# Optimization experiments

Measured on AMD Instinct MI355X. Metric: run time of the kernel, lower is better.

Reference implementation:

```python
import jax, jax.numpy as jnp
import numpy as np
import math

S, B, D, H = 2048, 2, 1024, 16
DK = D // H


def setup_inputs() -> dict:
    key = jax.random.key(0)
    ks = jax.random.split(key, 13)
    scale = 1.0 / math.sqrt(D)
    inp = {
        "query": jax.random.normal(ks[0], (S, B, D), jnp.float32),
        "key": jax.random.normal(ks[1], (S, B, D), jnp.float32),
        "value": jax.random.normal(ks[2], (S, B, D), jnp.float32),
        "mask": jax.random.normal(ks[3], (B, S, S), jnp.float32),
        # four Linear(d_model, d_model) layers: q, k, v, out. torch convention W:(out,in)
        "Wq": jax.random.normal(ks[4], (D, D), jnp.float32) * scale,
        "bq": jax.random.normal(ks[5], (D,), jnp.float32) * scale,
        "Wk": jax.random.normal(ks[6], (D, D), jnp.float32) * scale,
        "bk": jax.random.normal(ks[7], (D,), jnp.float32) * scale,
        "Wv": jax.random.normal(ks[8], (D, D), jnp.float32) * scale,
        "bv": jax.random.normal(ks[9], (D,), jnp.float32) * scale,
        "Wo": jax.random.normal(ks[10], (D, D), jnp.float32) * scale,
        "bo": jax.random.normal(ks[11], (D,), jnp.float32) * scale,
    }
    return inp


def reference(query, key, value, mask, Wq, bq, Wk, bk, Wv, bv, Wo, bo):
    # inputs are (tokens S, batch B, d_model D)
    def proj(x, W, b):  # torch Linear: x @ W.T + b, then split heads -> (B,H,S,DK)
        y = jnp.einsum('sbd,ed->sbe', x, W) + b
        return y.reshape(S, B, H, DK).transpose(1, 2, 0, 3)

    q = proj(query, Wq, bq)
    k = proj(key, Wk, bk)
    v = proj(value, Wv, bv)

    scores = jnp.einsum('bhsd,bhtd->bhst', q, k) / math.sqrt(DK)
    scores = scores + mask[:, None, :, :]  # broadcast over heads
    p_attn = jax.nn.softmax(scores, axis=-1)  # (B,H,S,S)

    x = jnp.einsum('bhst,bhtd->bhsd', p_attn, v)  # (B,H,S,DK)
    x = x.transpose(2, 0, 1, 3).reshape(S, B, D)  # (S,B,D)
    out = jnp.einsum('sbd,ed->sbe', x, Wo) + bo

    attn = p_attn.mean(axis=1)  # mean over heads -> (B,S,S)
    return out, attn
```

## Files before the change

kernel.cpp:

```cpp
#include <hip/hip_runtime.h>
#include <hip/hip_bf16.h>


#define S_LEN 2048
#define BATCH 2
#define DMODEL 1024
#define NH 16
#define DKH 64
#define SCALE 0.125f
#define QSCALE 0.180336878f
#define FMAX 20.0f
#define KSTRIDE 72

typedef __bf16 bf16_t;
typedef __attribute__((ext_vector_type(8))) __bf16 bf16x8;
typedef __attribute__((ext_vector_type(8))) unsigned short u16x8;
typedef __attribute__((ext_vector_type(4))) unsigned short u16x4;
typedef __attribute__((ext_vector_type(4))) float f32x4;

__device__ __forceinline__ unsigned short f32_bf16_rne(float f) {
  union { float f; unsigned int u; } v; v.f = f;
  unsigned int u = v.u;
  u += 0x7fffu + ((u >> 16) & 1u);
  return (unsigned short)(u >> 16);
}
__device__ __forceinline__ float bf16u_f32(unsigned short us) {
  union { unsigned int u; float f; } v; v.u = ((unsigned int)us) << 16;
  return v.f;
}
__device__ __forceinline__ f32x4 mfma_bf16(bf16x8 a, bf16x8 b, f32x4 c) {
  return __builtin_amdgcn_mfma_f32_16x16x32_bf16(a, b, c, 0, 0, 0);
}
__device__ __forceinline__ float exp2_fast(float x) {
#if __has_builtin(__builtin_amdgcn_exp2f)
  return __builtin_amdgcn_exp2f(x);
#else
  return __expf(x * 0.69314718f);
#endif
}
__device__ __forceinline__ unsigned int cvtpk(float lo, float hi) {
  unsigned int r;
  asm("v_cvt_pk_bf16_f32 %0, %1, %2" : "=v"(r) : "v"(lo), "v"(hi));
  return r;
}
__device__ __forceinline__ void gload16(const bf16_t* g, unsigned short* l) {
  __builtin_amdgcn_global_load_lds(
      (const __attribute__((address_space(1))) void*)g,
      (__attribute__((address_space(3))) void*)l, 16, 0, 0);
}

__global__ __launch_bounds__(256) void cvt_w_kernel(
    const float* __restrict__ w0, const float* __restrict__ w1,
    const float* __restrict__ w2, const float* __restrict__ w3,
    bf16_t* __restrict__ o0, bf16_t* __restrict__ o1,
    bf16_t* __restrict__ o2, bf16_t* __restrict__ o3) {
  const float* src; bf16_t* dst;
  switch (blockIdx.y) {
    case 0: src = w0; dst = o0; break;
    case 1: src = w1; dst = o1; break;
    case 2: src = w2; dst = o2; break;
    default: src = w3; dst = o3; break;
  }
  int i = (blockIdx.x * 256 + threadIdx.x) * 4;
  float4 v = *(const float4*)(src + i);
  union { unsigned short u[4]; uint2 q; } r;
  r.u[0] = f32_bf16_rne(v.x); r.u[1] = f32_bf16_rne(v.y);
  r.u[2] = f32_bf16_rne(v.z); r.u[3] = f32_bf16_rne(v.w);
  *(uint2*)(dst + i) = r.q;
}

__global__ __launch_bounds__(256) void cvt_x_kernel(
    const float* __restrict__ x0, const float* __restrict__ x1,
    const float* __restrict__ x2,
    bf16_t* __restrict__ o0, bf16_t* __restrict__ o1, bf16_t* __restrict__ o2) {
  const float* src; bf16_t* dst;
  switch (blockIdx.y) {
    case 0: src = x0; dst = o0; break;
    case 1: src = x1; dst = o1; break;
    default: src = x2; dst = o2; break;
  }
  int i = (blockIdx.x * 256 + threadIdx.x) * 4;
  float4 v = *(const float4*)(src + i);
  union { unsigned short u[4]; uint2 q; } r;
  r.u[0] = f32_bf16_rne(v.x); r.u[1] = f32_bf16_rne(v.y);
  r.u[2] = f32_bf16_rne(v.z); r.u[3] = f32_bf16_rne(v.w);
  *(uint2*)(dst + i) = r.q;
}

__global__ __launch_bounds__(256) void cvt_mask_kernel(
    const float* __restrict__ m, bf16_t* __restrict__ o) {
  int i = (blockIdx.x * 256 + threadIdx.x) * 4;
  float4 v = *(const float4*)(m + i);
  union { unsigned short u[4]; uint2 q; } r;
  r.u[0] = f32_bf16_rne(__expf(v.x - FMAX));
  r.u[1] = f32_bf16_rne(__expf(v.y - FMAX));
  r.u[2] = f32_bf16_rne(__expf(v.z - FMAX));
  r.u[3] = f32_bf16_rne(__expf(v.w - FMAX));
  *(uint2*)(o + i) = r.q;
}

__global__ __launch_bounds__(256) void proj_kernel(
    const bf16_t* __restrict__ Xq, const bf16_t* __restrict__ Xk, const bf16_t* __restrict__ Xv,
    const bf16_t* __restrict__ Wqb, const bf16_t* __restrict__ Wkb, const bf16_t* __restrict__ Wvb,
    const float* __restrict__ bq, const float* __restrict__ bk, const float* __restrict__ bv,
    bf16_t* __restrict__ qo, bf16_t* __restrict__ ko, bf16_t* __restrict__ vTo) {
  int mode = blockIdx.z;
  const bf16_t* X = (mode == 0) ? Xq : (mode == 1) ? Xk : Xv;
  const bf16_t* W = (mode == 0) ? Wqb : (mode == 1) ? Wkb : Wvb;
  const float* bias = (mode == 0) ? bq : (mode == 1) ? bk : bv;

  __shared__ __align__(16) unsigned short Alds[128 * 32];
  __shared__ __align__(16) unsigned short Blds[128 * 32];

  int tid = threadIdx.x;
  int wv = tid >> 6, lane = tid & 63, quad = lane >> 4, col = lane & 15;
  int wr = wv >> 1, wc = wv & 1;
  int rowbase = blockIdx.x * 128;
  int colbase = blockIdx.y * 128;

  int srow = tid >> 2;
  int sk8 = (tid & 3) * 8;
  const bf16_t* ga0 = X + (size_t)(rowbase + srow) * DMODEL + sk8;
  const bf16_t* gb0 = W + (size_t)(colbase + srow) * DMODEL + sk8;
  unsigned short* la0 = Alds + tid * 8;
  unsigned short* lb0 = Blds + tid * 8;

  f32x4 acc[4][4] = {};

  for (int k0 = 0; k0 < DMODEL; k0 += 32) {
    gload16(ga0 + k0, la0);
    gload16(ga0 + 64 * DMODEL + k0, la0 + 2048);
    gload16(gb0 + k0, lb0);
    gload16(gb0 + 64 * DMODEL + k0, lb0 + 2048);
    __syncthreads();

    union { u16x8 u; bf16x8 v; } af[4], bfr[4];
#pragma unroll
    for (int mi = 0; mi < 4; ++mi)
      af[mi].u = *(const u16x8*)(Alds + (wr * 64 + mi * 16 + col) * 32 + quad * 8);
#pragma unroll
    for (int ni = 0; ni < 4; ++ni)
      bfr[ni].u = *(const u16x8*)(Blds + (wc * 64 + ni * 16 + col) * 32 + quad * 8);
#pragma unroll
    for (int mi = 0; mi < 4; ++mi)
#pragma unroll
      for (int ni = 0; ni < 4; ++ni)
        acc[mi][ni] = mfma_bf16(af[mi].v, bfr[ni].v, acc[mi][ni]);
    __syncthreads();
  }

  float biasv[4];
#pragma unroll
  for (int ni = 0; ni < 4; ++ni)
    biasv[ni] = bias[colbase + wc * 64 + ni * 16 + col];

#pragma unroll
  for (int mi = 0; mi < 4; ++mi)
#pragma unroll
    for (int ni = 0; ni < 4; ++ni)
#pragma unroll
      for (int r = 0; r < 4; ++r) {
        int grow = rowbase + wr * 64 + mi * 16 + quad * 4 + r;
        int gcol = colbase + wc * 64 + ni * 16 + col;
        float val = acc[mi][ni][r] + biasv[ni];
        if (mode == 0) val *= QSCALE;
        unsigned short us = f32_bf16_rne(val);
        int s = grow >> 1, bb = grow & 1;
        int h = gcol >> 6, dk = gcol & 63;
        if (mode == 2) {
          ((unsigned short*)vTo)[((size_t)(bb * NH + h) * DKH + dk) * S_LEN + s] = us;
        } else {
          unsigned short* dst = (unsigned short*)(mode == 0 ? qo : ko);
          dst[((size_t)(bb * NH + h) * S_LEN + s) * DKH + dk] = us;
        }
      }
}

__global__ __launch_bounds__(256) void flash_kernel(
    const bf16_t* __restrict__ emb,
    const bf16_t* __restrict__ q_ws, const bf16_t* __restrict__ k_ws,
    const bf16_t* __restrict__ vT_ws,
    bf16_t* __restrict__ x_ws, float* __restrict__ rl_ws) {
  int tid = threadIdx.x;
  int w = tid >> 6, lane = tid & 63, quad = lane >> 4, col = lane & 15;

  int bid = blockIdx.x;
  int wi = bid >> 3;
  int bh = (bid & 7) * 4 + (wi & 3);
  int qblk = wi >> 2;
  int b = bh >> 4;
  int s0 = qblk * 128 + w * 32;
  int sA = s0, sB = s0 + 16;

  __shared__ __align__(16) unsigned short Klds[64 * KSTRIDE];
  __shared__ __align__(16) unsigned short Vlds[64 * KSTRIDE];

  const bf16_t* qh = q_ws + (size_t)bh * S_LEN * DKH;
  const bf16_t* kh = k_ws + (size_t)bh * S_LEN * DKH;
  const bf16_t* vh = vT_ws + (size_t)bh * DKH * S_LEN;
  const unsigned short* emA = (const unsigned short*)emb +
      (size_t)b * S_LEN * S_LEN + (size_t)(sA + col) * S_LEN;
  const unsigned short* emB = emA + (size_t)16 * S_LEN;

  bf16x8 qA0 = *(const bf16x8*)(qh + (sA + col) * DKH + quad * 8);
  bf16x8 qA1 = *(const bf16x8*)(qh + (sA + col) * DKH + 32 + quad * 8);
  bf16x8 qB0 = *(const bf16x8*)(qh + (sB + col) * DKH + quad * 8);
  bf16x8 qB1 = *(const bf16x8*)(qh + (sB + col) * DKH + 32 + quad * 8);

  int row1 = tid >> 3, row2 = row1 + 32;
  int ch = (tid & 7) * 8;
  int pi1 = (row1 & 32) + ((row1 & 16) >> 2) + ((row1 & 12) << 1) + (row1 & 3);
  int pi2 = (row2 & 32) + ((row2 & 16) >> 2) + ((row2 & 12) << 1) + (row2 & 3);
  const unsigned short* kg1 = (const unsigned short*)kh + (size_t)pi1 * DKH + ch;
  const unsigned short* kg2 = (const unsigned short*)kh + (size_t)pi2 * DKH + ch;
  const unsigned short* vg1 = (const unsigned short*)vh + (size_t)row1 * S_LEN + ch;
  const unsigned short* vg2 = (const unsigned short*)vh + (size_t)row2 * S_LEN + ch;
  u16x8* kl1 = (u16x8*)(Klds + row1 * KSTRIDE + ch);
  u16x8* kl2 = (u16x8*)(Klds + row2 * KSTRIDE + ch);
  u16x8* vl1 = (u16x8*)(Vlds + row1 * KSTRIDE + ch);
  u16x8* vl2 = (u16x8*)(Vlds + row2 * KSTRIDE + ch);

  f32x4 xA[4] = {}, xB[4] = {};
  float lsumA = 0.0f, lsumB = 0.0f;

  u16x8 kp1 = *(const u16x8*)kg1;
  u16x8 kp2 = *(const u16x8*)kg2;
  u16x8 vp1 = *(const u16x8*)vg1;
  u16x8 vp2 = *(const u16x8*)vg2;

  for (int t0 = 0; t0 < S_LEN; t0 += 64) {
    *kl1 = kp1; *kl2 = kp2; *vl1 = vp1; *vl2 = vp2;
    __syncthreads();

    if (t0 + 64 < S_LEN) {
      kp1 = *(const u16x8*)(kg1 + (size_t)(t0 + 64) * DKH);
      kp2 = *(const u16x8*)(kg2 + (size_t)(t0 + 64) * DKH);
      vp1 = *(const u16x8*)(vg1 + (t0 + 64));
      vp2 = *(const u16x8*)(vg2 + (t0 + 64));
    }

    u16x4 emA4[4], emB4[4];
#pragma unroll
    for (int j = 0; j < 4; ++j) {
      int f = t0 + ((j >> 1) << 5) + ((j & 1) << 2) + quad * 8;
      emA4[j] = *(const u16x4*)(emA + f);
      emB4[j] = *(const u16x4*)(emB + f);
    }

    f32x4 CA[4], CB[4];
#pragma unroll
    for (int j = 0; j < 4; ++j) {
      union { u16x8 u; bf16x8 v; } kb0, kb1;
      int row = j * 16 + col;
      kb0.u = *(const u16x8*)(Klds + row * KSTRIDE + quad * 8);
      kb1.u = *(const u16x8*)(Klds + row * KSTRIDE + 32 + quad * 8);
      f32x4 z = {};
      CA[j] = mfma_bf16(kb1.v, qA1, mfma_bf16(kb0.v, qA0, z));
      CB[j] = mfma_bf16(kb1.v, qB1, mfma_bf16(kb0.v, qB0, z));
    }

    unsigned int PA[8], PB[8];
#pragma unroll
    for (int j = 0; j < 4; ++j) {
      float a0 = exp2_fast(CA[j][0]) * bf16u_f32(emA4[j][0]);
      float a1 = exp2_fast(CA[j][1]) * bf16u_f32(emA4[j][1]);
      float a2 = exp2_fast(CA[j][2]) * bf16u_f32(emA4[j][2]);
      float a3 = exp2_fast(CA[j][3]) * bf16u_f32(emA4[j][3]);
      lsumA += (a0 + a1) + (a2 + a3);
      PA[j * 2] = cvtpk(a0, a1);
      PA[j * 2 + 1] = cvtpk(a2, a3);
      float b0 = exp2_fast(CB[j][0]) * bf16u_f32(emB4[j][0]);
      float b1 = exp2_fast(CB[j][1]) * bf16u_f32(emB4[j][1]);
      float b2 = exp2_fast(CB[j][2]) * bf16u_f32(emB4[j][2]);
      float b3 = exp2_fast(CB[j][3]) * bf16u_f32(emB4[j][3]);
      lsumB += (b0 + b1) + (b2 + b3);
      PB[j * 2] = cvtpk(b0, b1);
      PB[j * 2 + 1] = cvtpk(b2, b3);
    }
    union { unsigned int u32[4]; bf16x8 v; } bA0, bA1, bB0, bB1;
#pragma unroll
    for (int i = 0; i < 4; ++i) {
      bA0.u32[i] = PA[i]; bA1.u32[i] = PA[4 + i];
      bB0.u32[i] = PB[i]; bB1.u32[i] = PB[4 + i];
    }

#pragma unroll
    for (int ni = 0; ni < 4; ++ni) {
      union { u16x8 u; bf16x8 v; } vb0, vb1;
      int row = ni * 16 + col;
      vb0.u = *(const u16x8*)(Vlds + row * KSTRIDE + quad * 8);
      vb1.u = *(const u16x8*)(Vlds + row * KSTRIDE + 32 + quad * 8);
      xA[ni] = mfma_bf16(vb1.v, bA1.v, mfma_bf16(vb0.v, bA0.v, xA[ni]));
      xB[ni] = mfma_bf16(vb1.v, bB1.v, mfma_bf16(vb0.v, bB0.v, xB[ni]));
    }
    __syncthreads();
  }

  lsumA += __shfl_xor(lsumA, 16, 64); lsumA += __shfl_xor(lsumA, 32, 64);
  lsumB += __shfl_xor(lsumB, 16, 64); lsumB += __shfl_xor(lsumB, 32, 64);
  float rlA = 1.0f / lsumA, rlB = 1.0f / lsumB;

  unsigned short* xo = (unsigned short*)x_ws;
#pragma unroll
  for (int ni = 0; ni < 4; ++ni) {
    uint2 wa, wb;
    wa.x = cvtpk(xA[ni][0] * rlA, xA[ni][1] * rlA);
    wa.y = cvtpk(xA[ni][2] * rlA, xA[ni][3] * rlA);
    wb.x = cvtpk(xB[ni][0] * rlB, xB[ni][1] * rlB);
    wb.y = cvtpk(xB[ni][2] * rlB, xB[ni][3] * rlB);
    *(uint2*)(xo + ((size_t)bh * S_LEN + sA + col) * DKH + ni * 16 + quad * 4) = wa;
    *(uint2*)(xo + ((size_t)bh * S_LEN + sB + col) * DKH + ni * 16 + quad * 4) = wb;
  }
  if (quad == 0) {
    rl_ws[(size_t)bh * S_LEN + sA + col] = rlA;
    rl_ws[(size_t)bh * S_LEN + sB + col] = rlB;
  }
}

__global__ __launch_bounds__(512) void attn_kernel(
    const bf16_t* __restrict__ emb,
    const bf16_t* __restrict__ q_ws, const bf16_t* __restrict__ k_ws,
    const float* __restrict__ rl_ws,
    float* __restrict__ attn_out) {
  int tid = threadIdx.x;
  int w = tid >> 6, lane = tid & 63, quad = lane >> 4, col = lane & 15;
  int b = blockIdx.y;
  int s0 = blockIdx.x * 128 + w * 16;
  int t_base = blockIdx.z * 128;

  __shared__ __align__(16) unsigned short Klds[2][128 * 64];

  const unsigned short* emrow = (const unsigned short*)emb +
      (size_t)b * S_LEN * S_LEN + (size_t)(s0 + quad * 4) * S_LEN + t_base;
  float emf[8][4];
#pragma unroll
  for (int j = 0; j < 8; ++j)
#pragma unroll
    for (int r = 0; r < 4; ++r)
      emf[j][r] = bf16u_f32(emrow[r * S_LEN + j * 16 + col]);

  int srow = tid >> 3;
  int csw = ((tid & 7) ^ (srow & 7)) * 8;
  const bf16_t* kh0 = k_ws + (size_t)(b * NH) * S_LEN * DKH;
  const bf16_t* ks1 = kh0 + (size_t)(t_base + srow) * DKH + csw;
  const bf16_t* ks2 = kh0 + (size_t)(t_base + 64 + srow) * DKH + csw;

  const bf16_t* qp0 = q_ws + (size_t)(b * NH) * S_LEN * DKH + (size_t)(s0 + col) * DKH;
  const float* rlp = rl_ws + (size_t)(b * NH) * S_LEN + s0 + quad * 4;

  f32x4 acc[8] = {};

  gload16(ks1, &Klds[0][0] + tid * 8);
  gload16(ks2, &Klds[0][0] + 4096 + tid * 8);
  bf16x8 qf0c = *(const bf16x8*)(qp0 + quad * 8);
  bf16x8 qf1c = *(const bf16x8*)(qp0 + 32 + quad * 8);
  float rlc[4];
#pragma unroll
  for (int r = 0; r < 4; ++r) rlc[r] = rlp[r];
  __syncthreads();

  int cur = 0;
  for (int h = 0; h < NH; ++h) {
    bf16x8 qf0n = qf0c, qf1n = qf1c;
    float rln[4] = {rlc[0], rlc[1], rlc[2], rlc[3]};
    if (h + 1 < NH) {
      size_t off = (size_t)(h + 1) * S_LEN * DKH;
      unsigned short* dn = &Klds[cur ^ 1][0];
      gload16(ks1 + off, dn + tid * 8);
      gload16(ks2 + off, dn + 4096 + tid * 8);
      qf0n = *(const bf16x8*)(qp0 + off + quad * 8);
      qf1n = *(const bf16x8*)(qp0 + off + 32 + quad * 8);
      const float* rlh = rlp + (size_t)(h + 1) * S_LEN;
#pragma unroll
      for (int r = 0; r < 4; ++r) rln[r] = rlh[r];
    }

    const unsigned short* kb = &Klds[cur][0];
#pragma unroll
    for (int j = 0; j < 8; ++j) {
      int row = j * 16 + col;
      int rsw = row & 7;
      union { u16x8 u; bf16x8 v; } kb0, kb1;
      kb0.u = *(const u16x8*)(kb + row * 64 + ((quad ^ rsw) << 3));
      kb1.u = *(const u16x8*)(kb + row * 64 + (((quad + 4) ^ rsw) << 3));
      f32x4 z = {};
      f32x4 C = mfma_bf16(qf1c, kb1.v, mfma_bf16(qf0c, kb0.v, z));
#pragma unroll
      for (int r = 0; r < 4; ++r)
        acc[j][r] = fmaf(exp2_fast(C[r]), rlc[r], acc[j][r]);
    }
    __syncthreads();
    cur ^= 1;
    qf0c = qf0n; qf1c = qf1n;
#pragma unroll
    for (int r = 0; r < 4; ++r) rlc[r] = rln[r];
  }

#pragma unroll
  for (int j = 0; j < 8; ++j)
#pragma unroll
    for (int r = 0; r < 4; ++r)
      attn_out[((size_t)b * S_LEN + s0 + quad * 4 + r) * S_LEN + t_base + j * 16 + col] =
          acc[j][r] * emf[j][r] * (1.0f / NH);
}

__global__ __launch_bounds__(256) void outproj_kernel(
    const bf16_t* __restrict__ x_ws, const bf16_t* __restrict__ Wob,
    const float* __restrict__ bo, float* __restrict__ out) {
  __shared__ __align__(16) unsigned short Alds[128 * 32];
  __shared__ __align__(16) unsigned short Blds[128 * 32];

  int tid = threadIdx.x;
  int wv = tid >> 6, lane = tid & 63, quad = lane >> 4, col = lane & 15;
  int wr = wv >> 1, wc = wv & 1;
  int rowbase = blockIdx.x * 128;
  int colbase = blockIdx.y * 128;

  int srow = tid >> 2;
  int sk8 = (tid & 3) * 8;
  int r0 = rowbase + srow;
  int s0a = r0 >> 1, b0a = r0 & 1;
  int r1 = r0 + 64;
  int s1a = r1 >> 1, b1a = r1 & 1;
  const bf16_t* gb0 = Wob + (size_t)(colbase + srow) * DMODEL + sk8;
  unsigned short* la0 = Alds + tid * 8;
  unsigned short* lb0 = Blds + tid * 8;

  f32x4 acc[4][4] = {};

  for (int k0 = 0; k0 < DMODEL; k0 += 32) {
    int h = k0 >> 6, dk = (k0 & 63) + sk8;
    gload16(x_ws + ((size_t)(b0a * NH + h) * S_LEN + s0a) * DKH + dk, la0);
    gload16(x_ws + ((size_t)(b1a * NH + h) * S_LEN + s1a) * DKH + dk, la0 + 2048);
    gload16(gb0 + k0, lb0);
    gload16(gb0 + 64 * DMODEL + k0, lb0 + 2048);
    __syncthreads();

    union { u16x8 u; bf16x8 v; } af[4], bfr[4];
#pragma unroll
    for (int mi = 0; mi < 4; ++mi)
      af[mi].u = *(const u16x8*)(Alds + (wr * 64 + mi * 16 + col) * 32 + quad * 8);
#pragma unroll
    for (int ni = 0; ni < 4; ++ni)
      bfr[ni].u = *(const u16x8*)(Blds + (wc * 64 + ni * 16 + col) * 32 + quad * 8);
#pragma unroll
    for (int mi = 0; mi < 4; ++mi)
#pragma unroll
      for (int ni = 0; ni < 4; ++ni)
        acc[mi][ni] = mfma_bf16(af[mi].v, bfr[ni].v, acc[mi][ni]);
    __syncthreads();
  }

  float biasv[4];
#pragma unroll
  for (int ni = 0; ni < 4; ++ni)
    biasv[ni] = bo[colbase + wc * 64 + ni * 16 + col];

#pragma unroll
  for (int mi = 0; mi < 4; ++mi)
#pragma unroll
    for (int ni = 0; ni < 4; ++ni)
#pragma unroll
      for (int r = 0; r < 4; ++r) {
        int grow = rowbase + wr * 64 + mi * 16 + quad * 4 + r;
        int gcol = colbase + wc * 64 + ni * 16 + col;
        out[(size_t)grow * DMODEL + gcol] = acc[mi][ni][r] + biasv[ni];
      }
}

extern "C" void kernel_launch(void* const* d_in, const int* in_sizes, int n_in,
                              void* d_out, int out_size, void* d_ws, size_t ws_size,
                              hipStream_t stream) {
  const float* query = (const float*)d_in[0];
  const float* key_  = (const float*)d_in[1];
  const float* value = (const float*)d_in[2];
  const float* mask  = (const float*)d_in[3];
  const float* Wq = (const float*)d_in[4];
  const float* bq = (const float*)d_in[5];
  const float* Wk = (const float*)d_in[6];
  const float* bk = (const float*)d_in[7];
  const float* Wv = (const float*)d_in[8];
  const float* bv = (const float*)d_in[9];
  const float* Wo = (const float*)d_in[10];
  const float* bo = (const float*)d_in[11];

  char* ws = (char*)d_ws;
  bf16_t* q_ws  = (bf16_t*)(ws + 0);
  bf16_t* k_ws  = (bf16_t*)(ws + 8388608);
  bf16_t* vT_ws = (bf16_t*)(ws + 16777216);
  bf16_t* x_ws  = (bf16_t*)(ws + 25165824);
  float*  rl_ws = (float*)(ws + 33554432);
  bf16_t* Wqb = (bf16_t*)(ws + 33816576);
  bf16_t* Wkb = (bf16_t*)(ws + 35913728);
  bf16_t* Wvb = (bf16_t*)(ws + 38010880);
  bf16_t* Wob = (bf16_t*)(ws + 40108032);
  bf16_t* Xq_b = x_ws;
  bf16_t* Xk_b = (bf16_t*)(ws + 42205184);
  bf16_t* Xv_b = (bf16_t*)(ws + 50593792);
  bf16_t* emb  = (bf16_t*)(ws + 42205184);

  float* outp  = (float*)d_out;
  float* attnp = outp + (size_t)S_LEN * BATCH * DMODEL;

  cvt_w_kernel<<<dim3(1024, 4), 256, 0, stream>>>(Wq, Wk, Wv, Wo, Wqb, Wkb, Wvb, Wob);
  cvt_x_kernel<<<dim3(4096, 3), 256, 0, stream>>>(query, key_, value, Xq_b, Xk_b, Xv_b);
  proj_kernel<<<dim3(32, 8, 3), 256, 0, stream>>>(Xq_b, Xk_b, Xv_b,
                                                  Wqb, Wkb, Wvb, bq, bk, bv,
                                                  q_ws, k_ws, vT_ws);
  cvt_mask_kernel<<<dim3(8192), 256, 0, stream>>>(mask, emb);
  flash_kernel<<<dim3(512), 256, 0, stream>>>(emb, q_ws, k_ws, vT_ws, x_ws, rl_ws);
  attn_kernel<<<dim3(16, 2, 16), 512, 0, stream>>>(emb, q_ws, k_ws, rl_ws, attnp);
  outproj_kernel<<<dim3(32, 8), 256, 0, stream>>>(x_ws, Wob, bo, outp);
}
```

Before: 307.5 us.

## Double-buffer K/V tiles in LDS and compute row sums via MFMA with ones

The K/V tiles now use two LDS buffers, so each iteration writes the next tile while the current one is consumed, removing one __syncthreads per iteration. The softmax denominator is now accumulated with extra MFMAs against a vector of ones instead of scalar adds and cross-lane shuffles. This doubles LDS usage, which can lower occupancy. The row sums are taken from the bf16-rounded probabilities, so the denominator now matches the numerator's rounding but differs slightly from the earlier fp32 sum.

```diff
diff --git a/kernel.cpp b/kernel.cpp
--- a/kernel.cpp
+++ b/kernel.cpp
@@ -192,8 +192,8 @@
   int s0 = qblk * 128 + w * 32;
   int sA = s0, sB = s0 + 16;
 
-  __shared__ __align__(16) unsigned short Klds[64 * KSTRIDE];
-  __shared__ __align__(16) unsigned short Vlds[64 * KSTRIDE];
+  __shared__ __align__(16) unsigned short Klds[2][64 * KSTRIDE];
+  __shared__ __align__(16) unsigned short Vlds[2][64 * KSTRIDE];
 
   const bf16_t* qh = q_ws + (size_t)bh * S_LEN * DKH;
   const bf16_t* kh = k_ws + (size_t)bh * S_LEN * DKH;
@@ -206,6 +206,10 @@
   bf16x8 qA1 = *(const bf16x8*)(qh + (sA + col) * DKH + 32 + quad * 8);
   bf16x8 qB0 = *(const bf16x8*)(qh + (sB + col) * DKH + quad * 8);
   bf16x8 qB1 = *(const bf16x8*)(qh + (sB + col) * DKH + 32 + quad * 8);
+
+  union { unsigned short u[8]; bf16x8 v; } ones;
+#pragma unroll
+  for (int i = 0; i < 8; ++i) ones.u[i] = 0x3F80;
 
   int row1 = tid >> 3, row2 = row1 + 32;
   int ch = (tid & 7) * 8;
@@ -215,28 +219,43 @@
   const unsigned short* kg2 = (const unsigned short*)kh + (size_t)pi2 * DKH + ch;
   const unsigned short* vg1 = (const unsigned short*)vh + (size_t)row1 * S_LEN + ch;
   const unsigned short* vg2 = (const unsigned short*)vh + (size_t)row2 * S_LEN + ch;
-  u16x8* kl1 = (u16x8*)(Klds + row1 * KSTRIDE + ch);
-  u16x8* kl2 = (u16x8*)(Klds + row2 * KSTRIDE + ch);
-  u16x8* vl1 = (u16x8*)(Vlds + row1 * KSTRIDE + ch);
-  u16x8* vl2 = (u16x8*)(Vlds + row2 * KSTRIDE + ch);
 
   f32x4 xA[4] = {}, xB[4] = {};
-  float lsumA = 0.0f, lsumB = 0.0f;
+  f32x4 lsA = {}, lsB = {};
 
   u16x8 kp1 = *(const u16x8*)kg1;
   u16x8 kp2 = *(const u16x8*)kg2;
   u16x8 vp1 = *(const u16x8*)vg1;
   u16x8 vp2 = *(const u16x8*)vg2;
-
+  {
+    unsigned short* Kn = &Klds[0][0];
+    unsigned short* Vn = &Vlds[0][0];
+    *(u16x8*)(Kn + row1 * KSTRIDE + ch) = kp1;
+    *(u16x8*)(Kn + row2 * KSTRIDE + ch) = kp2;
+    *(u16x8*)(Vn + row1 * KSTRIDE + ch) = vp1;
+    *(u16x8*)(Vn + row2 * KSTRIDE + ch) = vp2;
+  }
+  kp1 = *(const u16x8*)(kg1 + (size_t)64 * DKH);
+  kp2 = *(const u16x8*)(kg2 + (size_t)64 * DKH);
+  vp1 = *(const u16x8*)(vg1 + 64);
+  vp2 = *(const u16x8*)(vg2 + 64);
+  __syncthreads();
+
+  int cur = 0;
   for (int t0 = 0; t0 < S_LEN; t0 += 64) {
-    *kl1 = kp1; *kl2 = kp2; *vl1 = vp1; *vl2 = vp2;
-    __syncthreads();
-
     if (t0 + 64 < S_LEN) {
-      kp1 = *(const u16x8*)(kg1 + (size_t)(t0 + 64) * DKH);
-      kp2 = *(const u16x8*)(kg2 + (size_t)(t0 + 64) * DKH);
-      vp1 = *(const u16x8*)(vg1 + (t0 + 64));
-      vp2 = *(const u16x8*)(vg2 + (t0 + 64));
+      unsigned short* Kn = &Klds[cur ^ 1][0];
+      unsigned short* Vn = &Vlds[cur ^ 1][0];
+      *(u16x8*)(Kn + row1 * KSTRIDE + ch) = kp1;
+      *(u16x8*)(Kn + row2 * KSTRIDE + ch) = kp2;
+      *(u16x8*)(Vn + row1 * KSTRIDE + ch) = vp1;
+      *(u16x8*)(Vn + row2 * KSTRIDE + ch) = vp2;
+      if (t0 + 128 < S_LEN) {
+        kp1 = *(const u16x8*)(kg1 + (size_t)(t0 + 128) * DKH);
+        kp2 = *(const u16x8*)(kg2 + (size_t)(t0 + 128) * DKH);
+        vp1 = *(const u16x8*)(vg1 + (t0 + 128));
+        vp2 = *(const u16x8*)(vg2 + (t0 + 128));
+      }
     }
 
     u16x4 emA4[4], emB4[4];
@@ -247,13 +266,15 @@
       emB4[j] = *(const u16x4*)(emB + f);
     }
 
+    const unsigned short* Kc = &Klds[cur][0];
+    const unsigned short* Vc = &Vlds[cur][0];
     f32x4 CA[4], CB[4];
 #pragma unroll
     for (int j = 0; j < 4; ++j) {
       union { u16x8 u; bf16x8 v; } kb0, kb1;
       int row = j * 16 + col;
-      kb0.u = *(const u16x8*)(Klds + row * KSTRIDE + quad * 8);
-      kb1.u = *(const u16x8*)(Klds + row * KSTRIDE + 32 + quad * 8);
+      kb0.u = *(const u16x8*)(Kc + row * KSTRIDE + quad * 8);
+      kb1.u = *(const u16x8*)(Kc + row * KSTRIDE + 32 + quad * 8);
       f32x4 z = {};
       CA[j] = mfma_bf16(kb1.v, qA1, mfma_bf16(kb0.v, qA0, z));
       CB[j] = mfma_bf16(kb1.v, qB1, mfma_bf16(kb0.v, qB0, z));
@@ -266,14 +287,12 @@
       float a1 = exp2_fast(CA[j][1]) * bf16u_f32(emA4[j][1]);
       float a2 = exp2_fast(CA[j][2]) * bf16u_f32(emA4[j][2]);
       float a3 = exp2_fast(CA[j][3]) * bf16u_f32(emA4[j][3]);
-      lsumA += (a0 + a1) + (a2 + a3);
       PA[j * 2] = cvtpk(a0, a1);
       PA[j * 2 + 1] = cvtpk(a2, a3);
       float b0 = exp2_fast(CB[j][0]) * bf16u_f32(emB4[j][0]);
       float b1 = exp2_fast(CB[j][1]) * bf16u_f32(emB4[j][1]);
       float b2 = exp2_fast(CB[j][2]) * bf16u_f32(emB4[j][2]);
       float b3 = exp2_fast(CB[j][3]) * bf16u_f32(emB4[j][3]);
-      lsumB += (b0 + b1) + (b2 + b3);
       PB[j * 2] = cvtpk(b0, b1);
       PB[j * 2 + 1] = cvtpk(b2, b3);
     }
@@ -284,21 +303,23 @@
       bB0.u32[i] = PB[i]; bB1.u32[i] = PB[4 + i];
     }
 
+    lsA = mfma_bf16(ones.v, bA1.v, mfma_bf16(ones.v, bA0.v, lsA));
+    lsB = mfma_bf16(ones.v, bB1.v, mfma_bf16(ones.v, bB0.v, lsB));
+
 #pragma unroll
     for (int ni = 0; ni < 4; ++ni) {
       union { u16x8 u; bf16x8 v; } vb0, vb1;
       int row = ni * 16 + col;
-      vb0.u = *(const u16x8*)(Vlds + row * KSTRIDE + quad * 8);
-      vb1.u = *(const u16x8*)(Vlds + row * KSTRIDE + 32 + quad * 8);
+      vb0.u = *(const u16x8*)(Vc + row * KSTRIDE + quad * 8);
+      vb1.u = *(const u16x8*)(Vc + row * KSTRIDE + 32 + quad * 8);
       xA[ni] = mfma_bf16(vb1.v, bA1.v, mfma_bf16(vb0.v, bA0.v, xA[ni]));
       xB[ni] = mfma_bf16(vb1.v, bB1.v, mfma_bf16(vb0.v, bB0.v, xB[ni]));
     }
     __syncthreads();
-  }
-
-  lsumA += __shfl_xor(lsumA, 16, 64); lsumA += __shfl_xor(lsumA, 32, 64);
-  lsumB += __shfl_xor(lsumB, 16, 64); lsumB += __shfl_xor(lsumB, 32, 64);
-  float rlA = 1.0f / lsumA, rlB = 1.0f / lsumB;
+    cur ^= 1;
+  }
+
+  float rlA = 1.0f / lsA[0], rlB = 1.0f / lsB[0];
 
   unsigned short* xo = (unsigned short*)x_ws;
 #pragma unroll
```

Result: no change. 311.3 us (+1.2%).
